# Kernel tuning notes

Hardware: AMD Instinct MI355X
Metric: run time of the kernel (lower is better)

Reference implementation:

```python
import jax, jax.numpy as jnp
import numpy as np

N = 40000      # nodes
E = 640000     # edges (avg degree 16)
F = 128        # num_features
D = 128        # embedding_size
G = 128        # graphs in batch


def _glorot(key, shape):
    fan_in = shape[-1]
    return jax.random.normal(key, shape, jnp.float32) / np.float32(np.sqrt(fan_in))


def setup_inputs() -> dict:
    key = jax.random.key(0)
    ks = jax.random.split(key, 20)
    inp = {
        "x": jax.random.normal(ks[0], (N, F), jnp.float32),
        "edge_index": jax.random.randint(ks[1], (2, E), 0, N, dtype=jnp.int32),
        "batch_index": jnp.sort(jax.random.randint(ks[2], (N,), 0, G, dtype=jnp.int32)),
    }
    dims = [(D, F), (D, D), (D, D), (D, D)]
    for i, (dout, din) in enumerate(dims):
        inp[f"Wroot{i}"] = _glorot(ks[3 + 3 * i], (dout, din))
        inp[f"Wrel{i}"] = _glorot(ks[4 + 3 * i], (dout, din))
        inp[f"b{i}"] = jnp.zeros((dout,), jnp.float32)
    inp["Wout"] = _glorot(ks[18], (1, D))
    inp["bout"] = jnp.zeros((1,), jnp.float32)
    return inp


def _graph_conv(h, src, dst, Wroot, Wrel, b, num_nodes):
    # PyG GraphConv (aggr='add'): out_i = W_root x_i + W_rel * sum_{j->i} x_j + b
    # Linear commutes with the sum, so aggregate first then one dense GEMM.
    agg = jax.ops.segment_sum(h[src], dst, num_segments=num_nodes)  # [N, din]
    return h @ Wroot.T + agg @ Wrel.T + b


def reference(x, edge_index, batch_index,
              Wroot0, Wrel0, b0, Wroot1, Wrel1, b1,
              Wroot2, Wrel2, b2, Wroot3, Wrel3, b3,
              Wout, bout):
    src, dst = edge_index[0], edge_index[1]
    n = x.shape[0]
    h = x.astype(jnp.float32)
    layers = [(Wroot0, Wrel0, b0), (Wroot1, Wrel1, b1),
              (Wroot2, Wrel2, b2), (Wroot3, Wrel3, b3)]
    for Wr, Wn, b in layers:
        h = jax.nn.gelu(_graph_conv(h, src, dst, Wr, Wn, b, n), approximate=False)
        # dropout p=0.5 -> identity at eval time
    # global mean pool over graphs (gap)
    sums = jax.ops.segment_sum(h, batch_index, num_segments=G)        # [G, D]
    counts = jax.ops.segment_sum(jnp.ones((n,), jnp.float32), batch_index, num_segments=G)
    pooled = sums / jnp.maximum(counts, 1.0)[:, None]
    return pooled @ Wout.T + bout  # [G, 1]
```

## Files before the change

### kernel.cpp

```cpp
#include <hip/hip_runtime.h>
#include <hip/hip_bf16.h>

typedef __bf16 bf16x8 __attribute__((ext_vector_type(8)));
typedef float  f32x4  __attribute__((ext_vector_type(4)));

__device__ __forceinline__ float blo(unsigned v) { return __uint_as_float(v << 16); }
__device__ __forceinline__ float bhi(unsigned v) { return __uint_as_float(v & 0xffff0000u); }
__device__ __forceinline__ unsigned short f2bf(float f) {
    unsigned u = __float_as_uint(f);
    u += 0x7fffu + ((u >> 16) & 1u);
    return (unsigned short)(u >> 16);
}
__device__ __forceinline__ float gelu_f(float x) {
    float t = 0.7978845608028654f * (x + 0.044715f * x * x * x);
    float e = __expf(2.0f * t);
    float th = 1.0f - 2.0f / (1.0f + e);
    return 0.5f * x * (1.0f + th);
}


__global__ void degree_kernel(const int* __restrict__ dst, int* __restrict__ deg, int E) {
    int e = blockIdx.x * blockDim.x + threadIdx.x;
    if (e < E) atomicAdd(&deg[dst[e]], 1);
}

__global__ void chunk_sum_kernel(const int* __restrict__ deg, int* __restrict__ bsum, int n) {
    int i = blockIdx.x * 1024 + threadIdx.x;
    int v = (i < n) ? deg[i] : 0;
#pragma unroll
    for (int m = 1; m < 64; m <<= 1) v += __shfl_xor(v, m, 64);
    __shared__ int ws[16];
    int wave = threadIdx.x >> 6, lane = threadIdx.x & 63;
    if (lane == 0) ws[wave] = v;
    __syncthreads();
    if (threadIdx.x == 0) {
        int s = 0;
#pragma unroll
        for (int k = 0; k < 16; ++k) s += ws[k];
        bsum[blockIdx.x] = s;
    }
}

__global__ void chunk_scan_kernel(const int* __restrict__ bsum, int* __restrict__ bbase,
                                  int nb, int* __restrict__ offsets, int n, int E) {
    int lane = threadIdx.x;
    int v = (lane < nb) ? bsum[lane] : 0;
    int s = v;
#pragma unroll
    for (int m = 1; m < 64; m <<= 1) {
        int t = __shfl_up(s, m, 64);
        if (lane >= m) s += t;
    }
    if (lane < nb) bbase[lane] = s - v;
    if (lane == 0) offsets[n] = E;
}

__global__ void scan_apply_kernel(const int* __restrict__ deg, const int* __restrict__ bbase,
                                  int* __restrict__ offsets, int* __restrict__ cursor, int n) {
    int i = blockIdx.x * 1024 + threadIdx.x;
    int lane = threadIdx.x & 63, wave = threadIdx.x >> 6;
    int v = (i < n) ? deg[i] : 0;
    int s = v;
#pragma unroll
    for (int m = 1; m < 64; m <<= 1) {
        int t = __shfl_up(s, m, 64);
        if (lane >= m) s += t;
    }
    __shared__ int ws[16];
    if (lane == 63) ws[wave] = s;
    __syncthreads();
    if (wave == 0 && lane < 16) {
        int wv = ws[lane];
        int ss = wv;
#pragma unroll
        for (int m = 1; m < 16; m <<= 1) {
            int t = __shfl_up(ss, m, 64);
            if (lane >= m) ss += t;
        }
        ws[lane] = ss - wv;
    }
    __syncthreads();
    int excl = (s - v) + ws[wave] + bbase[blockIdx.x];
    if (i < n) { offsets[i] = excl; cursor[i] = excl; }
}

__global__ void scatter_kernel(const int* __restrict__ src, const int* __restrict__ dst,
                               int* __restrict__ cursor, int* __restrict__ sorted_src, int E) {
    int e = blockIdx.x * blockDim.x + threadIdx.x;
    if (e < E) {
        int d = dst[e];
        int pos = atomicAdd(&cursor[d], 1);
        sorted_src[pos] = src[e];
    }
}

__global__ void bounds_kernel(const int* __restrict__ batch, int* __restrict__ gstart,
                              int N, int G) {
    int g = blockIdx.x * blockDim.x + threadIdx.x;
    if (g <= G) {
        int lo = 0, hi = N;
        while (lo < hi) {
            int mid = (lo + hi) >> 1;
            if (batch[mid] < g) lo = mid + 1; else hi = mid;
        }
        gstart[g] = lo;
    }
}

__global__ void cvt_kernel(const float4* __restrict__ in, ushort4* __restrict__ out, int n4) {
    int i = blockIdx.x * blockDim.x + threadIdx.x;
    if (i < n4) {
        float4 f = in[i];
        ushort4 o; o.x = f2bf(f.x); o.y = f2bf(f.y); o.z = f2bf(f.z); o.w = f2bf(f.w);
        out[i] = o;
    }
}

__global__ void build_wcat(const float* __restrict__ Wr, const float* __restrict__ Wn,
                           __hip_bfloat16* __restrict__ Wcat) {
    int idx = blockIdx.x * blockDim.x + threadIdx.x;
    if (idx < 128 * 256) {
        int j = idx >> 8, k = idx & 255;
        float v = (k < 128) ? Wr[j * 128 + k] : Wn[j * 128 + (k - 128)];
        Wcat[idx] = __float2bfloat16(v);
    }
}


__global__ void agg_kernel(const __hip_bfloat16* __restrict__ h,
                           const int* __restrict__ offsets,
                           const int* __restrict__ sorted_src,
                           __hip_bfloat16* __restrict__ agg, int N) {
    int node = blockIdx.x * 4 + (threadIdx.x >> 6);
    int lane = threadIdx.x & 63;
    if (node >= N) return;
    int s = offsets[node], e = offsets[node + 1];
    int half = lane >> 5, fl = lane & 31;
    const uint2* hu = (const uint2*)h;
    f32x4 A0 = {0,0,0,0}, A1 = {0,0,0,0}, A2 = {0,0,0,0}, A3 = {0,0,0,0};
    int t = s;
    for (; t + 8 <= e; t += 8) {
        int j0 = sorted_src[t + half];
        int j1 = sorted_src[t + 2 + half];
        int j2 = sorted_src[t + 4 + half];
        int j3 = sorted_src[t + 6 + half];
        uint2 v0 = hu[(size_t)j0 * 32 + fl];
        uint2 v1 = hu[(size_t)j1 * 32 + fl];
        uint2 v2 = hu[(size_t)j2 * 32 + fl];
        uint2 v3 = hu[(size_t)j3 * 32 + fl];
        A0[0] += blo(v0.x); A0[1] += bhi(v0.x); A0[2] += blo(v0.y); A0[3] += bhi(v0.y);
        A1[0] += blo(v1.x); A1[1] += bhi(v1.x); A1[2] += blo(v1.y); A1[3] += bhi(v1.y);
        A2[0] += blo(v2.x); A2[1] += bhi(v2.x); A2[2] += blo(v2.y); A2[3] += bhi(v2.y);
        A3[0] += blo(v3.x); A3[1] += bhi(v3.x); A3[2] += blo(v3.y); A3[3] += bhi(v3.y);
    }
    if (t + 4 <= e) {
        int j0 = sorted_src[t + half];
        int j1 = sorted_src[t + 2 + half];
        uint2 v0 = hu[(size_t)j0 * 32 + fl];
        uint2 v1 = hu[(size_t)j1 * 32 + fl];
        A0[0] += blo(v0.x); A0[1] += bhi(v0.x); A0[2] += blo(v0.y); A0[3] += bhi(v0.y);
        A1[0] += blo(v1.x); A1[1] += bhi(v1.x); A1[2] += blo(v1.y); A1[3] += bhi(v1.y);
        t += 4;
    }
    if (t + 2 <= e) {
        int j0 = sorted_src[t + half];
        uint2 v0 = hu[(size_t)j0 * 32 + fl];
        A0[0] += blo(v0.x); A0[1] += bhi(v0.x); A0[2] += blo(v0.y); A0[3] += bhi(v0.y);
        t += 2;
    }
    if (t < e && half == 0) {
        int j = sorted_src[t];
        uint2 v = hu[(size_t)j * 32 + fl];
        A1[0] += blo(v.x); A1[1] += bhi(v.x); A1[2] += blo(v.y); A1[3] += bhi(v.y);
    }
    f32x4 A;
#pragma unroll
    for (int q = 0; q < 4; ++q) {
        float a = (A0[q] + A1[q]) + (A2[q] + A3[q]);
        a += __shfl_xor(a, 32, 64);
        A[q] = a;
    }
    if (half == 0) {
        ushort4 o; o.x = f2bf(A[0]); o.y = f2bf(A[1]); o.z = f2bf(A[2]); o.w = f2bf(A[3]);
        *reinterpret_cast<ushort4*>(&agg[(size_t)node * 128 + fl * 4]) = o;
    }
}

__global__ __launch_bounds__(512, 4)
void gemm_layer_kernel(const __hip_bfloat16* __restrict__ h,
                       const __hip_bfloat16* __restrict__ agg,
                       const __hip_bfloat16* __restrict__ Wcat,
                       const float* __restrict__ bias,
                       __hip_bfloat16* __restrict__ out, int N) {
    int wave = threadIdx.x >> 6;
    int lane = threadIdx.x & 63;
    int row0 = blockIdx.x * 64;
    int la  = lane & 15;
    int ke0 = (lane >> 4) * 8;
    int col = wave * 16 + la;

    bf16x8 b[8];
#pragma unroll
    for (int ks = 0; ks < 8; ++ks)
        b[ks] = *reinterpret_cast<const bf16x8*>(&Wcat[(size_t)col * 256 + ks * 32 + ke0]);
    float bv = bias[col];

    f32x4 acc[4];
#pragma unroll
    for (int m = 0; m < 4; ++m) {
        int r = row0 + m * 16 + la;
        if (r >= N) r = N - 1;
        const __hip_bfloat16* hr = &h[(size_t)r * 128];
        const __hip_bfloat16* ar = &agg[(size_t)r * 128];
        bf16x8 a[8];
#pragma unroll
        for (int ks = 0; ks < 4; ++ks) {
            a[ks]     = *reinterpret_cast<const bf16x8*>(&hr[ks * 32 + ke0]);
            a[ks + 4] = *reinterpret_cast<const bf16x8*>(&ar[ks * 32 + ke0]);
        }
        f32x4 c = {0, 0, 0, 0};
#pragma unroll
        for (int ks = 0; ks < 8; ++ks)
            c = __builtin_amdgcn_mfma_f32_16x16x32_bf16(a[ks], b[ks], c, 0, 0, 0);
        acc[m] = c;
    }

    int r0 = row0 + (lane >> 4) * 4;
#pragma unroll
    for (int m = 0; m < 4; ++m) {
#pragma unroll
        for (int j = 0; j < 4; ++j) {
            int r = r0 + m * 16 + j;
            if (r < N)
                out[(size_t)r * 128 + col] = __float2bfloat16(gelu_f(acc[m][j] + bv));
        }
    }
}

__global__ void pool_partial(const __hip_bfloat16* __restrict__ h,
                             const int* __restrict__ batch,
                             const float* __restrict__ Wout,
                             float* __restrict__ outsum, int N) {
    int wid = blockIdx.x * 4 + (threadIdx.x >> 6);
    int lane = threadIdx.x & 63;
    int i0 = wid * 16;
    if (i0 >= N) return;
    int half = lane >> 5, fl = lane & 31;
    const uint2* hu = (const uint2*)h;
    float w0 = Wout[4 * fl], w1 = Wout[4 * fl + 1];
    float w2 = Wout[4 * fl + 2], w3 = Wout[4 * fl + 3];
    float dot = 0.f;
    int cur = -1;
#pragma unroll
    for (int t = 0; t < 8; ++t) {
        int i = i0 + 2 * t + half;
        if (i < N) {
            int g = batch[i];
            uint2 v = hu[(size_t)i * 32 + fl];
            float d = blo(v.x) * w0 + bhi(v.x) * w1 + blo(v.y) * w2 + bhi(v.y) * w3;
            if (g != cur) {
                if (cur >= 0) {
                    float r = dot;
#pragma unroll
                    for (int m = 16; m >= 1; m >>= 1) r += __shfl_xor(r, m, 64);
                    if (fl == 0) atomicAdd(&outsum[cur], r);
                }
                cur = g; dot = d;
            } else {
                dot += d;
            }
        }
    }
    if (cur >= 0) {
        float r = dot;
#pragma unroll
        for (int m = 16; m >= 1; m >>= 1) r += __shfl_xor(r, m, 64);
        if (fl == 0) atomicAdd(&outsum[cur], r);
    }
}

__global__ void pool_finish(const float* __restrict__ outsum,
                            const int* __restrict__ gstart,
                            const float* __restrict__ bout,
                            float* __restrict__ out, int G) {
    int g = blockIdx.x * blockDim.x + threadIdx.x;
    if (g < G) {
        float cnt = (float)(gstart[g + 1] - gstart[g]);
        out[g] = outsum[g] / fmaxf(cnt, 1.0f) + bout[0];
    }
}


extern "C" void kernel_launch(void* const* d_in, const int* in_sizes, int n_in,
                              void* d_out, int out_size, void* d_ws, size_t ws_size,
                              hipStream_t stream) {
    const float* x          = (const float*)d_in[0];
    const int*   edge_index = (const int*)d_in[1];
    const int*   batch      = (const int*)d_in[2];
    const float* Wroot[4] = {(const float*)d_in[3], (const float*)d_in[6],
                             (const float*)d_in[9], (const float*)d_in[12]};
    const float* Wrel[4]  = {(const float*)d_in[4], (const float*)d_in[7],
                             (const float*)d_in[10], (const float*)d_in[13]};
    const float* bias[4]  = {(const float*)d_in[5], (const float*)d_in[8],
                             (const float*)d_in[11], (const float*)d_in[14]};
    const float* Wout = (const float*)d_in[15];
    const float* bout = (const float*)d_in[16];
    float* out = (float*)d_out;

    const int N = in_sizes[2];
    const int E = in_sizes[1] / 2;
    const int G = 128;
    const int* src = edge_index;
    const int* dst = edge_index + E;

    char* ws = (char*)d_ws;
    size_t o = 0;
    auto alloc = [&](size_t bytes) { void* p = ws + o; o += (bytes + 255) & ~(size_t)255; return p; };

    __hip_bfloat16* hx   = (__hip_bfloat16*)alloc((size_t)N * 128 * 2);
    __hip_bfloat16* hb0  = (__hip_bfloat16*)alloc((size_t)N * 128 * 2);
    __hip_bfloat16* hb1  = (__hip_bfloat16*)alloc((size_t)N * 128 * 2);
    __hip_bfloat16* agg  = (__hip_bfloat16*)alloc((size_t)N * 128 * 2);
    __hip_bfloat16* wcat[4];
    for (int l = 0; l < 4; ++l) wcat[l] = (__hip_bfloat16*)alloc(128 * 256 * 2);
    int* deg     = (int*)alloc((size_t)N * 4);
    int* offsets = (int*)alloc((size_t)(N + 1) * 4);
    int* cursor  = (int*)alloc((size_t)N * 4);
    int* sorted  = (int*)alloc((size_t)E * 4);
    int* gstart  = (int*)alloc((size_t)(G + 1) * 4);
    int* bsum    = (int*)alloc(64 * 4);
    int* bbase   = (int*)alloc(64 * 4);
    float* outsum = (float*)alloc((size_t)G * 4);

    const int nb = (N + 1023) / 1024;

    hipMemsetAsync(deg, 0, (size_t)N * 4, stream);
    degree_kernel<<<(E + 255) / 256, 256, 0, stream>>>(dst, deg, E);
    chunk_sum_kernel<<<nb, 1024, 0, stream>>>(deg, bsum, N);
    chunk_scan_kernel<<<1, 64, 0, stream>>>(bsum, bbase, nb, offsets, N, E);
    scan_apply_kernel<<<nb, 1024, 0, stream>>>(deg, bbase, offsets, cursor, N);
    scatter_kernel<<<(E + 255) / 256, 256, 0, stream>>>(src, dst, cursor, sorted, E);
    bounds_kernel<<<1, 256, 0, stream>>>(batch, gstart, N, G);

    cvt_kernel<<<(N * 128 / 4 + 255) / 256, 256, 0, stream>>>(
        (const float4*)x, (ushort4*)hx, N * 128 / 4);
    for (int l = 0; l < 4; ++l)
        build_wcat<<<(128 * 256 + 255) / 256, 256, 0, stream>>>(Wroot[l], Wrel[l], wcat[l]);

    __hip_bfloat16* hin = hx;
    __hip_bfloat16* houts[4] = {hb0, hb1, hb0, hb1};
    for (int l = 0; l < 4; ++l) {
        agg_kernel<<<(N + 3) / 4, 256, 0, stream>>>(hin, offsets, sorted, agg, N);
        gemm_layer_kernel<<<(N + 63) / 64, 512, 0, stream>>>(hin, agg, wcat[l], bias[l], houts[l], N);
        hin = houts[l];
    }

    hipMemsetAsync(outsum, 0, (size_t)G * 4, stream);
    pool_partial<<<((N + 15) / 16 + 3) / 4, 256, 0, stream>>>(hin, batch, Wout, outsum, N);
    pool_finish<<<1, 128, 0, stream>>>(outsum, gstart, bout, out, G);
}
```

Before: 427.0 us.

## Fuse neighbor aggregation into GEMM layer kernel via LDS staging

```diff
diff --git a/kernel.cpp b/kernel.cpp
--- a/kernel.cpp
+++ b/kernel.cpp
@@ -116,87 +116,93 @@
     }
 }
 
-__global__ void build_wcat(const float* __restrict__ Wr, const float* __restrict__ Wn,
-                           __hip_bfloat16* __restrict__ Wcat) {
+__global__ void build_wcat_all(const float* __restrict__ Wr0, const float* __restrict__ Wn0,
+                               const float* __restrict__ Wr1, const float* __restrict__ Wn1,
+                               const float* __restrict__ Wr2, const float* __restrict__ Wn2,
+                               const float* __restrict__ Wr3, const float* __restrict__ Wn3,
+                               __hip_bfloat16* __restrict__ wcat) {
     int idx = blockIdx.x * blockDim.x + threadIdx.x;
-    if (idx < 128 * 256) {
-        int j = idx >> 8, k = idx & 255;
-        float v = (k < 128) ? Wr[j * 128 + k] : Wn[j * 128 + (k - 128)];
-        Wcat[idx] = __float2bfloat16(v);
-    }
-}
-
-
-__global__ void agg_kernel(const __hip_bfloat16* __restrict__ h,
-                           const int* __restrict__ offsets,
-                           const int* __restrict__ sorted_src,
-                           __hip_bfloat16* __restrict__ agg, int N) {
-    int node = blockIdx.x * 4 + (threadIdx.x >> 6);
-    int lane = threadIdx.x & 63;
-    if (node >= N) return;
-    int s = offsets[node], e = offsets[node + 1];
-    int half = lane >> 5, fl = lane & 31;
-    const uint2* hu = (const uint2*)h;
-    f32x4 A0 = {0,0,0,0}, A1 = {0,0,0,0}, A2 = {0,0,0,0}, A3 = {0,0,0,0};
-    int t = s;
-    for (; t + 8 <= e; t += 8) {
-        int j0 = sorted_src[t + half];
-        int j1 = sorted_src[t + 2 + half];
-        int j2 = sorted_src[t + 4 + half];
-        int j3 = sorted_src[t + 6 + half];
-        uint2 v0 = hu[(size_t)j0 * 32 + fl];
-        uint2 v1 = hu[(size_t)j1 * 32 + fl];
-        uint2 v2 = hu[(size_t)j2 * 32 + fl];
-        uint2 v3 = hu[(size_t)j3 * 32 + fl];
-        A0[0] += blo(v0.x); A0[1] += bhi(v0.x); A0[2] += blo(v0.y); A0[3] += bhi(v0.y);
-        A1[0] += blo(v1.x); A1[1] += bhi(v1.x); A1[2] += blo(v1.y); A1[3] += bhi(v1.y);
-        A2[0] += blo(v2.x); A2[1] += bhi(v2.x); A2[2] += blo(v2.y); A2[3] += bhi(v2.y);
-        A3[0] += blo(v3.x); A3[1] += bhi(v3.x); A3[2] += blo(v3.y); A3[3] += bhi(v3.y);
-    }
-    if (t + 4 <= e) {
-        int j0 = sorted_src[t + half];
-        int j1 = sorted_src[t + 2 + half];
-        uint2 v0 = hu[(size_t)j0 * 32 + fl];
-        uint2 v1 = hu[(size_t)j1 * 32 + fl];
-        A0[0] += blo(v0.x); A0[1] += bhi(v0.x); A0[2] += blo(v0.y); A0[3] += bhi(v0.y);
-        A1[0] += blo(v1.x); A1[1] += bhi(v1.x); A1[2] += blo(v1.y); A1[3] += bhi(v1.y);
-        t += 4;
-    }
-    if (t + 2 <= e) {
-        int j0 = sorted_src[t + half];
-        uint2 v0 = hu[(size_t)j0 * 32 + fl];
-        A0[0] += blo(v0.x); A0[1] += bhi(v0.x); A0[2] += blo(v0.y); A0[3] += bhi(v0.y);
-        t += 2;
-    }
-    if (t < e && half == 0) {
-        int j = sorted_src[t];
-        uint2 v = hu[(size_t)j * 32 + fl];
-        A1[0] += blo(v.x); A1[1] += bhi(v.x); A1[2] += blo(v.y); A1[3] += bhi(v.y);
-    }
-    f32x4 A;
-#pragma unroll
-    for (int q = 0; q < 4; ++q) {
-        float a = (A0[q] + A1[q]) + (A2[q] + A3[q]);
-        a += __shfl_xor(a, 32, 64);
-        A[q] = a;
-    }
-    if (half == 0) {
-        ushort4 o; o.x = f2bf(A[0]); o.y = f2bf(A[1]); o.z = f2bf(A[2]); o.w = f2bf(A[3]);
-        *reinterpret_cast<ushort4*>(&agg[(size_t)node * 128 + fl * 4]) = o;
-    }
-}
-
+    if (idx >= 4 * 128 * 256) return;
+    int l = idx >> 15;
+    int j = (idx >> 8) & 127, k = idx & 255;
+    const float* Wr = (l == 0) ? Wr0 : (l == 1) ? Wr1 : (l == 2) ? Wr2 : Wr3;
+    const float* Wn = (l == 0) ? Wn0 : (l == 1) ? Wn1 : (l == 2) ? Wn2 : Wn3;
+    float v = (k < 128) ? Wr[j * 128 + k] : Wn[j * 128 + (k - 128)];
+    wcat[idx] = __float2bfloat16(v);
+}
+
+#define LDS_STRIDE 264
 __global__ __launch_bounds__(512, 4)
-void gemm_layer_kernel(const __hip_bfloat16* __restrict__ h,
-                       const __hip_bfloat16* __restrict__ agg,
-                       const __hip_bfloat16* __restrict__ Wcat,
-                       const float* __restrict__ bias,
-                       __hip_bfloat16* __restrict__ out, int N) {
+void layer_kernel(const __hip_bfloat16* __restrict__ h,
+                  const int* __restrict__ offsets,
+                  const int* __restrict__ sorted_src,
+                  const __hip_bfloat16* __restrict__ Wcat,
+                  const float* __restrict__ bias,
+                  __hip_bfloat16* __restrict__ out, int N) {
+    __shared__ char lds[64 * LDS_STRIDE];
     int wave = threadIdx.x >> 6;
     int lane = threadIdx.x & 63;
     int row0 = blockIdx.x * 64;
+    int half = lane >> 5, fl = lane & 31;
+    const uint2* hu = (const uint2*)h;
+
+#pragma unroll 1
+    for (int i = 0; i < 8; ++i) {
+        int lr = wave * 8 + i;
+        int node = row0 + lr;
+        if (node < N) {
+            int s = offsets[node], e = offsets[node + 1];
+            f32x4 A0 = {0,0,0,0}, A1 = {0,0,0,0}, A2 = {0,0,0,0}, A3 = {0,0,0,0};
+            int t = s;
+            for (; t + 8 <= e; t += 8) {
+                int j0 = sorted_src[t + half];
+                int j1 = sorted_src[t + 2 + half];
+                int j2 = sorted_src[t + 4 + half];
+                int j3 = sorted_src[t + 6 + half];
+                uint2 v0 = hu[(size_t)j0 * 32 + fl];
+                uint2 v1 = hu[(size_t)j1 * 32 + fl];
+                uint2 v2 = hu[(size_t)j2 * 32 + fl];
+                uint2 v3 = hu[(size_t)j3 * 32 + fl];
+                A0[0] += blo(v0.x); A0[1] += bhi(v0.x); A0[2] += blo(v0.y); A0[3] += bhi(v0.y);
+                A1[0] += blo(v1.x); A1[1] += bhi(v1.x); A1[2] += blo(v1.y); A1[3] += bhi(v1.y);
+                A2[0] += blo(v2.x); A2[1] += bhi(v2.x); A2[2] += blo(v2.y); A2[3] += bhi(v2.y);
+                A3[0] += blo(v3.x); A3[1] += bhi(v3.x); A3[2] += blo(v3.y); A3[3] += bhi(v3.y);
+            }
+            if (t + 4 <= e) {
+                int j0 = sorted_src[t + half];
+                int j1 = sorted_src[t + 2 + half];
+                uint2 v0 = hu[(size_t)j0 * 32 + fl];
+                uint2 v1 = hu[(size_t)j1 * 32 + fl];
+                A0[0] += blo(v0.x); A0[1] += bhi(v0.x); A0[2] += blo(v0.y); A0[3] += bhi(v0.y);
+                A1[0] += blo(v1.x); A1[1] += bhi(v1.x); A1[2] += blo(v1.y); A1[3] += bhi(v1.y);
+                t += 4;
+            }
+            if (t + 2 <= e) {
+                int j0 = sorted_src[t + half];
+                uint2 v0 = hu[(size_t)j0 * 32 + fl];
+                A0[0] += blo(v0.x); A0[1] += bhi(v0.x); A0[2] += blo(v0.y); A0[3] += bhi(v0.y);
+                t += 2;
+            }
+            if (t < e && half == 0) {
+                int j = sorted_src[t];
+                uint2 v = hu[(size_t)j * 32 + fl];
+                A1[0] += blo(v.x); A1[1] += bhi(v.x); A1[2] += blo(v.y); A1[3] += bhi(v.y);
+            }
+            float q0 = (A0[0] + A1[0]) + (A2[0] + A3[0]); q0 += __shfl_xor(q0, 32, 64);
+            float q1 = (A0[1] + A1[1]) + (A2[1] + A3[1]); q1 += __shfl_xor(q1, 32, 64);
+            float q2 = (A0[2] + A1[2]) + (A2[2] + A3[2]); q2 += __shfl_xor(q2, 32, 64);
+            float q3 = (A0[3] + A1[3]) + (A2[3] + A3[3]); q3 += __shfl_xor(q3, 32, 64);
+            if (half == 0) {
+                ushort4 o; o.x = f2bf(q0); o.y = f2bf(q1); o.z = f2bf(q2); o.w = f2bf(q3);
+                *reinterpret_cast<ushort4*>(&lds[lr * LDS_STRIDE + fl * 8]) = o;
+            }
+        }
+    }
+    __syncthreads();
+
     int la  = lane & 15;
-    int ke0 = (lane >> 4) * 8;
+    int keg = lane >> 4;
+    int ke0 = keg * 8;
     int col = wave * 16 + la;
 
     bf16x8 b[8];
@@ -211,13 +217,14 @@
         int r = row0 + m * 16 + la;
         if (r >= N) r = N - 1;
         const __hip_bfloat16* hr = &h[(size_t)r * 128];
-        const __hip_bfloat16* ar = &agg[(size_t)r * 128];
         bf16x8 a[8];
 #pragma unroll
-        for (int ks = 0; ks < 4; ++ks) {
-            a[ks]     = *reinterpret_cast<const bf16x8*>(&hr[ks * 32 + ke0]);
-            a[ks + 4] = *reinterpret_cast<const bf16x8*>(&ar[ks * 32 + ke0]);
-        }
+        for (int ks = 0; ks < 4; ++ks)
+            a[ks] = *reinterpret_cast<const bf16x8*>(&hr[ks * 32 + ke0]);
+#pragma unroll
+        for (int ks = 0; ks < 4; ++ks)
+            a[ks + 4] = *reinterpret_cast<const bf16x8*>(
+                &lds[(m * 16 + la) * LDS_STRIDE + ks * 64 + keg * 16]);
         f32x4 c = {0, 0, 0, 0};
 #pragma unroll
         for (int ks = 0; ks < 8; ++ks)
@@ -236,6 +243,7 @@
         }
     }
 }
+
 
 __global__ void pool_partial(const __hip_bfloat16* __restrict__ h,
                              const int* __restrict__ batch,
@@ -320,9 +328,7 @@
     __hip_bfloat16* hx   = (__hip_bfloat16*)alloc((size_t)N * 128 * 2);
     __hip_bfloat16* hb0  = (__hip_bfloat16*)alloc((size_t)N * 128 * 2);
     __hip_bfloat16* hb1  = (__hip_bfloat16*)alloc((size_t)N * 128 * 2);
-    __hip_bfloat16* agg  = (__hip_bfloat16*)alloc((size_t)N * 128 * 2);
-    __hip_bfloat16* wcat[4];
-    for (int l = 0; l < 4; ++l) wcat[l] = (__hip_bfloat16*)alloc(128 * 256 * 2);
+    __hip_bfloat16* wcat = (__hip_bfloat16*)alloc((size_t)4 * 128 * 256 * 2);
     int* deg     = (int*)alloc((size_t)N * 4);
     int* offsets = (int*)alloc((size_t)(N + 1) * 4);
     int* cursor  = (int*)alloc((size_t)N * 4);
@@ -344,14 +350,14 @@
 
     cvt_kernel<<<(N * 128 / 4 + 255) / 256, 256, 0, stream>>>(
         (const float4*)x, (ushort4*)hx, N * 128 / 4);
-    for (int l = 0; l < 4; ++l)
-        build_wcat<<<(128 * 256 + 255) / 256, 256, 0, stream>>>(Wroot[l], Wrel[l], wcat[l]);
+    build_wcat_all<<<(4 * 128 * 256 + 255) / 256, 256, 0, stream>>>(
+        Wroot[0], Wrel[0], Wroot[1], Wrel[1], Wroot[2], Wrel[2], Wroot[3], Wrel[3], wcat);
 
     __hip_bfloat16* hin = hx;
     __hip_bfloat16* houts[4] = {hb0, hb1, hb0, hb1};
     for (int l = 0; l < 4; ++l) {
-        agg_kernel<<<(N + 3) / 4, 256, 0, stream>>>(hin, offsets, sorted, agg, N);
-        gemm_layer_kernel<<<(N + 63) / 64, 512, 0, stream>>>(hin, agg, wcat[l], bias[l], houts[l], N);
+        layer_kernel<<<(N + 63) / 64, 512, 0, stream>>>(
+            hin, offsets, sorted, wcat + (size_t)l * 128 * 256, bias[l], houts[l], N);
         hin = houts[l];
     }
 
```

After: 399.4 us. 1.07x faster.
